# Kernel optimization log

Hardware: AMD Instinct MI355X
Metric: run time of the kernel (lower is better)

The kernel has to match this reference:

```python
import jax, jax.numpy as jnp
import numpy as np

N, E = 50000, 800000
IN_DIM, HID, HEADS, OUT_DIM = 128, 64, 4, 40
NEG_SLOPE = 0.2


def setup_inputs() -> dict:
    key = jax.random.key(0)
    ks = jax.random.split(key, 12)
    x = jax.random.normal(ks[0], (N, IN_DIM), dtype=jnp.float32)
    edge_index = jax.random.randint(ks[1], (2, E), 0, N, dtype=jnp.int64)
    timesteps = jax.random.randint(ks[2], (N,), 0, 100, dtype=jnp.int64)
    s = 1.0 / np.sqrt(IN_DIM)
    W_proj = jax.random.uniform(ks[3], (IN_DIM, HID), jnp.float32, -s, s)
    b_proj = jnp.zeros((HID,), jnp.float32)
    time_emb = jax.random.normal(ks[4], (100, HID), dtype=jnp.float32)
    sg = 1.0 / np.sqrt(HID)
    W_gat = jax.random.uniform(ks[5], (HID, HEADS * HID), jnp.float32, -sg, sg)
    att_src = jax.random.uniform(ks[6], (HEADS, HID), jnp.float32, -sg, sg)
    att_dst = jax.random.uniform(ks[7], (HEADS, HID), jnp.float32, -sg, sg)
    b_gat = jnp.zeros((HEADS * HID,), jnp.float32)
    sc = 1.0 / np.sqrt(HEADS * HID)
    W_cls = jax.random.uniform(ks[8], (HEADS * HID, OUT_DIM), jnp.float32, -sc, sc)
    b_cls = jnp.zeros((OUT_DIM,), jnp.float32)
    return {"x": x, "edge_index": edge_index, "timesteps": timesteps,
            "W_proj": W_proj, "b_proj": b_proj, "time_emb": time_emb,
            "W_gat": W_gat, "att_src": att_src, "att_dst": att_dst, "b_gat": b_gat,
            "W_cls": W_cls, "b_cls": b_cls}


def reference(x, edge_index, timesteps, W_proj, b_proj, time_emb,
              W_gat, att_src, att_dst, b_gat, W_cls, b_cls):
    n = x.shape[0]
    # feature projection + ReLU + time embedding
    h0 = jax.nn.relu(x @ W_proj + b_proj) + time_emb[timesteps]  # [N, HID]
    # --- GATConv (PyG semantics, add_self_loops=True, concat heads) ---
    h = (h0 @ W_gat).reshape(n, HEADS, HID)              # [N, H, C]
    a_src = jnp.einsum('nhc,hc->nh', h, att_src)         # [N, H]
    a_dst = jnp.einsum('nhc,hc->nh', h, att_dst)
    loops = jnp.arange(n, dtype=edge_index.dtype)
    src = jnp.concatenate([edge_index[0], loops])        # [E+N]
    dst = jnp.concatenate([edge_index[1], loops])
    e = jax.nn.leaky_relu(a_src[src] + a_dst[dst], NEG_SLOPE)  # [E+N, H]
    # segment softmax over incoming edges per destination node
    m = jax.ops.segment_max(e, dst, num_segments=n)      # [N, H]
    p = jnp.exp(e - m[dst])
    denom = jax.ops.segment_sum(p, dst, num_segments=n)  # [N, H]
    alpha = p / (denom[dst] + 1e-16)                     # [E+N, H]
    msg = alpha[:, :, None] * h[src]                     # [E+N, H, C]
    agg = jax.ops.segment_sum(msg, dst, num_segments=n)  # [N, H, C]
    gat_out = agg.reshape(n, HEADS * HID) + b_gat
    # ReLU + (dropout is identity in eval) + classifier
    return jax.nn.relu(gat_out) @ W_cls + b_cls          # [N, OUT_DIM]
```

## Files before the change

kernel.cpp:

```cpp
#include <hip/hip_runtime.h>
#include <hip/hip_fp16.h>

#define IN_DIM 128
#define HID 64
#define HEADS 4
#define OUT_DIM 40
#define CAP 64
#define NEG 0.2f
#define PA_EPB 4096
#define BKT_SH 9
#define BKT_CAP 10240
#define GPAD 264

__device__ __forceinline__ float lrelu(float v) { return v > 0.f ? v : NEG * v; }

union HU { float2 f2; __half2 h2[2]; };
union HU2 { float4 f4; __half2 h2[4]; };

typedef _Float16 h2v __attribute__((ext_vector_type(2)));
union DU { float4 f4; h2v h[4]; };

typedef _Float16 f16x8 __attribute__((ext_vector_type(8)));
typedef float f32x4 __attribute__((ext_vector_type(4)));
union FU { float4 f4; f16x8 v; };

__device__ __forceinline__ float4 unpack_h4(float2 bits) {
    HU u; u.f2 = bits;
    float2 lo = __half22float2(u.h2[0]);
    float2 hi = __half22float2(u.h2[1]);
    return make_float4(lo.x, lo.y, hi.x, hi.y);
}

__global__ __launch_bounds__(256) void partA_kernel(
    const int* __restrict__ ei, int E, int nbkt, int paBlocks,
    int* __restrict__ cnt, unsigned int* __restrict__ ebuf,
    const float* __restrict__ Wg, const float* __restrict__ attS,
    const float* __restrict__ attD, const float* __restrict__ Wc,
    float* __restrict__ aSf, float* __restrict__ aDf,
    __half* __restrict__ WgT, __half* __restrict__ WcTg)
{
    if (blockIdx.x >= paBlocks) {
        int gid = (blockIdx.x - paBlocks) * 256 + threadIdx.x;
        if (gid < 256) {
            int k = gid >> 2, hd = gid & 3;
            const float* wr = Wg + k * 256 + hd * 64;
            const float* as = attS + hd * 64;
            const float* ad = attD + hd * 64;
            float ss = 0.f, dd = 0.f;
            for (int c = 0; c < 64; ++c) { float w = wr[c]; ss += w * as[c]; dd += w * ad[c]; }
            aSf[k * 4 + hd] = ss;
            aDf[k * 4 + hd] = dd;
        } else if (gid < 256 + 256 * HID) {
            int i = gid - 256;
            int o = i >> 6, k = i & 63;
            WgT[i] = __float2half(Wg[k * 256 + o]);
        } else if (gid < 256 + 256 * HID + OUT_DIM * 256) {
            int i = gid - 256 - 256 * HID;
            int o = i >> 8, k = i & 255;
            WcTg[i] = __float2half(Wc[k * OUT_DIM + o]);
        }
        return;
    }

    __shared__ int localCnt[128];
    __shared__ int baseArr[128];
    for (int i = threadIdx.x; i < nbkt; i += 256) localCnt[i] = 0;
    __syncthreads();

    const int e0 = blockIdx.x * PA_EPB + threadIdx.x;
    unsigned short l[16];
#pragma unroll
    for (int j = 0; j < 16; ++j) {
        int e = e0 + j * 256;
        if (e < E) {
            int d = ei[E + e];
            l[j] = (unsigned short)atomicAdd(&localCnt[d >> BKT_SH], 1);
        }
    }
    __syncthreads();
    for (int i = threadIdx.x; i < nbkt; i += 256)
        baseArr[i] = atomicAdd(&cnt[i], localCnt[i]);
    __syncthreads();
#pragma unroll
    for (int j = 0; j < 16; ++j) {
        int e = e0 + j * 256;
        if (e < E) {
            int s = ei[e];
            int d = ei[E + e];
            int b = d >> BKT_SH;
            int off = baseArr[b] + (int)l[j];
            if (off < BKT_CAP)
                ebuf[(size_t)b * BKT_CAP + off] =
                    ((unsigned)(d & ((1 << BKT_SH) - 1)) << 16) | (unsigned)s;
        }
    }
}

__global__ __launch_bounds__(256) void partB_kernel(
    const unsigned int* __restrict__ ebuf, const int* __restrict__ cnt,
    int* __restrict__ deg, unsigned short* __restrict__ csr, int N)
{
    __shared__ int cntL[512];
    __shared__ unsigned short rows[512 * CAP];
    const int b = blockIdx.x;
    for (int i = threadIdx.x; i < 512; i += 256) cntL[i] = 0;
    __syncthreads();

    int cb = cnt[b]; cb = cb < BKT_CAP ? cb : BKT_CAP;
    const unsigned int* eb = ebuf + (size_t)b * BKT_CAP;
    for (int i = threadIdx.x; i < cb; i += 256) {
        unsigned v = eb[i];
        int dloc = v >> 16;
        int slot = atomicAdd(&cntL[dloc], 1);
        if (slot < CAP) rows[dloc * CAP + slot] = (unsigned short)(v & 0xFFFFu);
    }
    __syncthreads();

    const int d0 = b << BKT_SH;
    for (int i = threadIdx.x; i < 512; i += 256) {
        int d = d0 + i;
        if (d < N) deg[d] = cntL[i];
    }
    int limRows = N - d0; limRows = limRows < 512 ? limRows : 512;
    if (limRows <= 0) return;
    const uint4* rsrc = (const uint4*)rows;
    uint4* rdst = (uint4*)(csr + (size_t)d0 * CAP);
    int nvec = (limRows * CAP) >> 3;
    for (int i = threadIdx.x; i < nvec; i += 256)
        rdst[i] = rsrc[i];
}

__global__ __launch_bounds__(256) void proj_kernel(
    const float* __restrict__ x, const float* __restrict__ Wp,
    const float* __restrict__ bp, const float* __restrict__ temb,
    const int* __restrict__ ts, const float* __restrict__ aSf,
    const float* __restrict__ aDf,
    __half* __restrict__ h0h, float* __restrict__ aS, float* __restrict__ aD, int N)
{
    __shared__ __half Wl[IN_DIM * HID];
    for (int i = threadIdx.x * 8; i < IN_DIM * HID; i += 256 * 8) {
        float4 wa = *(const float4*)(Wp + i);
        float4 wb = *(const float4*)(Wp + i + 4);
        HU2 u;
        u.h2[0] = __floats2half2_rn(wa.x, wa.y);
        u.h2[1] = __floats2half2_rn(wa.z, wa.w);
        u.h2[2] = __floats2half2_rn(wb.x, wb.y);
        u.h2[3] = __floats2half2_rn(wb.z, wb.w);
        *(float4*)(Wl + i) = u.f4;
    }
    __syncthreads();

    const int t = threadIdx.x;
    const int lane = t & 63, wq = t >> 6;
    const int cg = lane & 15, ng = lane >> 4;
    const int c0 = cg * 4;
    const int nodeBase = blockIdx.x * 32 + wq * 8 + ng * 2;

    float4 acc[2];
#pragma unroll
    for (int j = 0; j < 2; ++j) acc[j] = make_float4(0.f, 0.f, 0.f, 0.f);

    for (int k0 = 0; k0 < IN_DIM; k0 += 4) {
        float4 xv[2];
#pragma unroll
        for (int j = 0; j < 2; ++j) {
            int n = nodeBase + j; n = n < N ? n : N - 1;
            xv[j] = *(const float4*)(x + (size_t)n * IN_DIM + k0);
        }
        float4 wv[4];
#pragma unroll
        for (int kk = 0; kk < 4; ++kk)
            wv[kk] = unpack_h4(*(const float2*)(Wl + (k0 + kk) * HID + c0));
#pragma unroll
        for (int j = 0; j < 2; ++j) {
            const float* xs = (const float*)&xv[j];
#pragma unroll
            for (int kk = 0; kk < 4; ++kk) {
                acc[j].x += xs[kk] * wv[kk].x;
                acc[j].y += xs[kk] * wv[kk].y;
                acc[j].z += xs[kk] * wv[kk].z;
                acc[j].w += xs[kk] * wv[kk].w;
            }
        }
    }
    const float4 bb = *(const float4*)(bp + c0);
    float4 s0 = *(const float4*)(aSf + (c0 + 0) * 4);
    float4 s1 = *(const float4*)(aSf + (c0 + 1) * 4);
    float4 s2 = *(const float4*)(aSf + (c0 + 2) * 4);
    float4 s3 = *(const float4*)(aSf + (c0 + 3) * 4);
    float4 d0 = *(const float4*)(aDf + (c0 + 0) * 4);
    float4 d1 = *(const float4*)(aDf + (c0 + 1) * 4);
    float4 d2 = *(const float4*)(aDf + (c0 + 2) * 4);
    float4 d3 = *(const float4*)(aDf + (c0 + 3) * 4);
#pragma unroll
    for (int j = 0; j < 2; ++j) {
        int n = nodeBase + j;
        float4 r = make_float4(0.f, 0.f, 0.f, 0.f);
        if (n < N) {
            int tv = ts[n];
            float4 te = *(const float4*)(temb + (size_t)tv * HID + c0);
            r.x = fmaxf(acc[j].x + bb.x, 0.f) + te.x;
            r.y = fmaxf(acc[j].y + bb.y, 0.f) + te.y;
            r.z = fmaxf(acc[j].z + bb.z, 0.f) + te.z;
            r.w = fmaxf(acc[j].w + bb.w, 0.f) + te.w;
            HU u;
            u.h2[0] = __floats2half2_rn(r.x, r.y);
            u.h2[1] = __floats2half2_rn(r.z, r.w);
            *(float2*)(h0h + (size_t)n * HID + c0) = u.f2;
        }
        float4 pS, pD;
        pS.x = r.x * s0.x + r.y * s1.x + r.z * s2.x + r.w * s3.x;
        pS.y = r.x * s0.y + r.y * s1.y + r.z * s2.y + r.w * s3.y;
        pS.z = r.x * s0.z + r.y * s1.z + r.z * s2.z + r.w * s3.z;
        pS.w = r.x * s0.w + r.y * s1.w + r.z * s2.w + r.w * s3.w;
        pD.x = r.x * d0.x + r.y * d1.x + r.z * d2.x + r.w * d3.x;
        pD.y = r.x * d0.y + r.y * d1.y + r.z * d2.y + r.w * d3.y;
        pD.z = r.x * d0.z + r.y * d1.z + r.z * d2.z + r.w * d3.z;
        pD.w = r.x * d0.w + r.y * d1.w + r.z * d2.w + r.w * d3.w;
#pragma unroll
        for (int off = 8; off > 0; off >>= 1) {
            pS.x += __shfl_down(pS.x, off); pS.y += __shfl_down(pS.y, off);
            pS.z += __shfl_down(pS.z, off); pS.w += __shfl_down(pS.w, off);
            pD.x += __shfl_down(pD.x, off); pD.y += __shfl_down(pD.y, off);
            pD.z += __shfl_down(pD.z, off); pD.w += __shfl_down(pD.w, off);
        }
        if (cg == 0 && n < N) {
            *(float4*)(aS + (size_t)n * 4) = pS;
            *(float4*)(aD + (size_t)n * 4) = pD;
        }
    }
}

__global__ __launch_bounds__(256) void agg_kernel(
    const __half* __restrict__ h0h, const float* __restrict__ aS,
    const float* __restrict__ aD, const int* __restrict__ deg,
    const unsigned short* __restrict__ csr, __half* __restrict__ agg0h, int N)
{
    __shared__ float p_lds[4 * CAP * HEADS];
    __shared__ int   s_lds[4 * CAP];

    const int t = threadIdx.x;
    const int lane = t & 63, wq = t >> 6;
    const int n = blockIdx.x * 4 + wq;
    if (n >= N) return;
    const int hd16 = lane >> 4, li = lane & 15;

    const float adn = aD[n * 4 + hd16];
    const float es = lrelu(aS[n * 4 + hd16] + adn);

    int dn = deg[n]; dn = dn < CAP ? dn : CAP;
    const unsigned short* cs = csr + (size_t)n * CAP;
    float* pL = p_lds + wq * CAP * HEADS;
    int*   sL = s_lds + wq * CAP;

    float m = -1e30f;
    for (int i = li; i < dn; i += 16) {
        int src = cs[i];
        if (hd16 == 0) sL[i] = src << 7;
        float e = lrelu(aS[src * 4 + hd16] + adn);
        pL[i * HEADS + hd16] = e;
        m = fmaxf(m, e);
    }
#pragma unroll
    for (int off = 8; off > 0; off >>= 1)
        m = fmaxf(m, __shfl_xor(m, off));
    m = fmaxf(m, es);
    float mh[4], esh[4];
#pragma unroll
    for (int h = 0; h < 4; ++h) {
        mh[h]  = __shfl(m, h * 16);
        esh[h] = __shfl(es, h * 16);
    }

    float sp = 0.f;
    for (int idx = lane; idx < dn * 4; idx += 64) {
        float p = __expf(pL[idx] - mh[idx & 3]);
        pL[idx] = p;
        sp += p;
    }
#pragma unroll
    for (int off = 4; off < 64; off <<= 1)
        sp += __shfl_xor(sp, off);
    float pselfh[4], invh[4];
#pragma unroll
    for (int h = 0; h < 4; ++h) {
        float sh = __shfl(sp, h);
        pselfh[h] = __expf(esh[h] - mh[h]);
        invh[h] = 1.f / (sh + pselfh[h] + 1e-16f);
    }

    const int half = lane >> 5;
    const int ch2 = lane & 31;
    const char* hb = (const char*)h0h;
    const int laneByte = ch2 << 2;

    float2 acc[4];
    {
        float lo = 0.f, hi = 0.f;
        if (half == 0) {
            __half2 v2 = *(const __half2*)(hb + ((size_t)n << 7) + laneByte);
            float2 f = __half22float2(v2);
            lo = f.x; hi = f.y;
        }
#pragma unroll
        for (int h = 0; h < 4; ++h) {
            acc[h].x = pselfh[h] * lo;
            acc[h].y = pselfh[h] * hi;
        }
    }
    int i = 0;
    for (; i + 8 <= dn; i += 8) {
        int off0 = sL[i + 0 + half];
        int off1 = sL[i + 2 + half];
        int off2 = sL[i + 4 + half];
        int off3 = sL[i + 6 + half];
        __half2 v0 = *(const __half2*)(hb + off0 + laneByte);
        __half2 v1 = *(const __half2*)(hb + off1 + laneByte);
        __half2 v2 = *(const __half2*)(hb + off2 + laneByte);
        __half2 v3 = *(const __half2*)(hb + off3 + laneByte);
        float4 p0 = *(const float4*)(pL + (i + 0 + half) * 4);
        float4 p1 = *(const float4*)(pL + (i + 2 + half) * 4);
        float4 p2 = *(const float4*)(pL + (i + 4 + half) * 4);
        float4 p3 = *(const float4*)(pL + (i + 6 + half) * 4);
        float2 f;
        f = __half22float2(v0);
        acc[0].x += p0.x * f.x; acc[0].y += p0.x * f.y;
        acc[1].x += p0.y * f.x; acc[1].y += p0.y * f.y;
        acc[2].x += p0.z * f.x; acc[2].y += p0.z * f.y;
        acc[3].x += p0.w * f.x; acc[3].y += p0.w * f.y;
        f = __half22float2(v1);
        acc[0].x += p1.x * f.x; acc[0].y += p1.x * f.y;
        acc[1].x += p1.y * f.x; acc[1].y += p1.y * f.y;
        acc[2].x += p1.z * f.x; acc[2].y += p1.z * f.y;
        acc[3].x += p1.w * f.x; acc[3].y += p1.w * f.y;
        f = __half22float2(v2);
        acc[0].x += p2.x * f.x; acc[0].y += p2.x * f.y;
        acc[1].x += p2.y * f.x; acc[1].y += p2.y * f.y;
        acc[2].x += p2.z * f.x; acc[2].y += p2.z * f.y;
        acc[3].x += p2.w * f.x; acc[3].y += p2.w * f.y;
        f = __half22float2(v3);
        acc[0].x += p3.x * f.x; acc[0].y += p3.x * f.y;
        acc[1].x += p3.y * f.x; acc[1].y += p3.y * f.y;
        acc[2].x += p3.z * f.x; acc[2].y += p3.z * f.y;
        acc[3].x += p3.w * f.x; acc[3].y += p3.w * f.y;
    }
    for (; i + 2 <= dn; i += 2) {
        int off0 = sL[i + half];
        __half2 v0 = *(const __half2*)(hb + off0 + laneByte);
        float4 p0 = *(const float4*)(pL + (i + half) * 4);
        float2 f = __half22float2(v0);
        acc[0].x += p0.x * f.x; acc[0].y += p0.x * f.y;
        acc[1].x += p0.y * f.x; acc[1].y += p0.y * f.y;
        acc[2].x += p0.z * f.x; acc[2].y += p0.z * f.y;
        acc[3].x += p0.w * f.x; acc[3].y += p0.w * f.y;
    }
    if (i < dn && half == 0) {
        int off0 = sL[i];
        __half2 v0 = *(const __half2*)(hb + off0 + laneByte);
        float4 p0 = *(const float4*)(pL + i * 4);
        float2 f = __half22float2(v0);
        acc[0].x += p0.x * f.x; acc[0].y += p0.x * f.y;
        acc[1].x += p0.y * f.x; acc[1].y += p0.y * f.y;
        acc[2].x += p0.z * f.x; acc[2].y += p0.z * f.y;
        acc[3].x += p0.w * f.x; acc[3].y += p0.w * f.y;
    }
#pragma unroll
    for (int h = 0; h < 4; ++h) {
        acc[h].x += __shfl_xor(acc[h].x, 32);
        acc[h].y += __shfl_xor(acc[h].y, 32);
    }
    if (lane < 32) {
        __half2* dst = (__half2*)(agg0h + (size_t)n * 256);
#pragma unroll
        for (int h = 0; h < 4; ++h)
            dst[h * 32 + ch2] = __floats2half2_rn(acc[h].x * invh[h],
                                                  acc[h].y * invh[h]);
    }
}

__global__ __launch_bounds__(256) void gatcls_kernel(
    const __half* __restrict__ agg0h, const __half* __restrict__ WgT,
    const float* __restrict__ bg, const __half* __restrict__ WcTg,
    const float* __restrict__ bc, float* __restrict__ out, int N)
{
    __shared__ __half gtile[32 * GPAD];

    const int t = threadIdx.x;
    const int lane = t & 63, wq = t >> 6;
    const int m16 = lane & 15, quad = lane >> 4;
    const int nodeBase = blockIdx.x * 32;

    {
        const int h = wq;
        f32x4 acc[2][4];
#pragma unroll
        for (int mt = 0; mt < 2; ++mt)
#pragma unroll
            for (int nt = 0; nt < 4; ++nt)
                acc[mt][nt] = (f32x4){0.f, 0.f, 0.f, 0.f};

#pragma unroll
        for (int ks = 0; ks < 2; ++ks) {
            FU a[2], b[4];
#pragma unroll
            for (int mt = 0; mt < 2; ++mt) {
                int n = nodeBase + mt * 16 + m16; n = n < N ? n : N - 1;
                a[mt].f4 = *(const float4*)(agg0h + (size_t)n * 256 + h * 64 + ks * 32 + quad * 8);
            }
#pragma unroll
            for (int nt = 0; nt < 4; ++nt) {
                int o = h * 64 + nt * 16 + m16;
                b[nt].f4 = *(const float4*)(WgT + o * 64 + ks * 32 + quad * 8);
            }
#pragma unroll
            for (int mt = 0; mt < 2; ++mt)
#pragma unroll
                for (int nt = 0; nt < 4; ++nt)
                    acc[mt][nt] = __builtin_amdgcn_mfma_f32_16x16x32_f16(
                        a[mt].v, b[nt].v, acc[mt][nt], 0, 0, 0);
        }
#pragma unroll
        for (int nt = 0; nt < 4; ++nt) {
            int o = h * 64 + nt * 16 + m16;
            float bv = bg[o];
#pragma unroll
            for (int mt = 0; mt < 2; ++mt) {
#pragma unroll
                for (int r = 0; r < 4; ++r) {
                    int nloc = mt * 16 + quad * 4 + r;
                    gtile[nloc * GPAD + o] = __float2half(fmaxf(acc[mt][nt][r] + bv, 0.f));
                }
            }
        }
    }
    __syncthreads();

    {
        const int mt = wq >> 1;
        const int ntCount = (wq & 1) ? 1 : 2;
        const int ntBase = (wq & 1) ? 2 : 0;
        f32x4 acc2[2];
        acc2[0] = (f32x4){0.f, 0.f, 0.f, 0.f};
        acc2[1] = (f32x4){0.f, 0.f, 0.f, 0.f};
#pragma unroll
        for (int ks = 0; ks < 8; ++ks) {
            FU a; a.f4 = *(const float4*)(gtile + (mt * 16 + m16) * GPAD + ks * 32 + quad * 8);
            for (int q = 0; q < ntCount; ++q) {
                int o = (ntBase + q) * 16 + m16;
                int oc = o < OUT_DIM ? o : OUT_DIM - 1;
                FU b; b.f4 = *(const float4*)(WcTg + oc * 256 + ks * 32 + quad * 8);
                acc2[q] = __builtin_amdgcn_mfma_f32_16x16x32_f16(a.v, b.v, acc2[q], 0, 0, 0);
            }
        }
        for (int q = 0; q < ntCount; ++q) {
            int o = (ntBase + q) * 16 + m16;
            if (o < OUT_DIM) {
                float bv = bc[o];
#pragma unroll
                for (int r = 0; r < 4; ++r) {
                    int n = nodeBase + mt * 16 + quad * 4 + r;
                    if (n < N) out[(size_t)n * OUT_DIM + o] = acc2[q][r] + bv;
                }
            }
        }
    }
}

extern "C" void kernel_launch(void* const* d_in, const int* in_sizes, int n_in,
                              void* d_out, int out_size, void* d_ws, size_t ws_size,
                              hipStream_t stream) {
    const float* x    = (const float*)d_in[0];
    const int*   ei   = (const int*)d_in[1];
    const int*   ts   = (const int*)d_in[2];
    const float* Wp   = (const float*)d_in[3];
    const float* bp   = (const float*)d_in[4];
    const float* temb = (const float*)d_in[5];
    const float* Wg   = (const float*)d_in[6];
    const float* attS = (const float*)d_in[7];
    const float* attD = (const float*)d_in[8];
    const float* bg   = (const float*)d_in[9];
    const float* Wc   = (const float*)d_in[10];
    const float* bc   = (const float*)d_in[11];
    float* out = (float*)d_out;

    const int N = in_sizes[0] / IN_DIM;
    const int E = in_sizes[1] / 2;
    const int nbkt = (N + (1 << BKT_SH) - 1) >> BKT_SH;

    char* w = (char*)d_ws;
    __half*         h0h   = (__half*)w;         w += (size_t)N * HID * 2;
    __half*         agg0h = (__half*)w;         w += (size_t)N * 256 * 2;
    float*          aS    = (float*)w;          w += (size_t)N * HEADS * 4;
    float*          aD    = (float*)w;          w += (size_t)N * HEADS * 4;
    int*            deg   = (int*)w;            w += (size_t)N * 4;
    unsigned short* csr   = (unsigned short*)w; w += (size_t)N * CAP * 2;
    unsigned int*   ebuf  = (unsigned int*)w;   w += (size_t)nbkt * BKT_CAP * 4;
    int*            cnt   = (int*)w;            w += (size_t)nbkt * 4;
    float*          aSf   = (float*)w;          w += 256 * 4;
    float*          aDf   = (float*)w;          w += 256 * 4;
    __half*         WgT   = (__half*)w;         w += (size_t)256 * HID * 2;
    __half*         WcTg  = (__half*)w;         w += (size_t)OUT_DIM * 256 * 2;

    const int paBlocks = (E + PA_EPB - 1) / PA_EPB;
    const int prepWork = 256 + 256 * HID + OUT_DIM * 256;
    const int prepBlocks = (prepWork + 255) / 256;

    hipMemsetAsync(cnt, 0, (size_t)nbkt * 4, stream);
    partA_kernel<<<paBlocks + prepBlocks, 256, 0, stream>>>(
        ei, E, nbkt, paBlocks, cnt, ebuf, Wg, attS, attD, Wc, aSf, aDf, WgT, WcTg);
    partB_kernel<<<nbkt, 256, 0, stream>>>(ebuf, cnt, deg, csr, N);
    proj_kernel<<<(N + 31) / 32, 256, 0, stream>>>(x, Wp, bp, temb, ts, aSf, aDf,
                                                   h0h, aS, aD, N);
    agg_kernel<<<(N + 3) / 4, 256, 0, stream>>>(h0h, aS, aD, deg, csr, agg0h, N);
    gatcls_kernel<<<(N + 31) / 32, 256, 0, stream>>>(agg0h, WgT, bg, WcTg, bc, out, N);
}
```

Measured before the change: 210.9 us.

## Fuse CSR bucket build into projection kernel and scatter CSR directly to global

Merges the CSR bucket-fill kernel and the feature projection kernel into a single launch, where the first nbkt blocks build CSR rows and the remaining blocks do the projection. The bucket blocks now write each edge's source id straight to global CSR memory instead of staging a 64KB shared-memory row buffer and copying it out. This removes one launch boundary and lets the two independent phases overlap. In exchange, CSR writes become scattered 2-byte global stores, and the merged kernel's shared-memory footprint is sized to the projection weights.

```diff
diff --git a/kernel.cpp b/kernel.cpp
--- a/kernel.cpp
+++ b/kernel.cpp
@@ -96,48 +96,42 @@
     }
 }
 
-__global__ __launch_bounds__(256) void partB_kernel(
+__global__ __launch_bounds__(256) void partBproj_kernel(
     const unsigned int* __restrict__ ebuf, const int* __restrict__ cnt,
-    int* __restrict__ deg, unsigned short* __restrict__ csr, int N)
-{
-    __shared__ int cntL[512];
-    __shared__ unsigned short rows[512 * CAP];
-    const int b = blockIdx.x;
-    for (int i = threadIdx.x; i < 512; i += 256) cntL[i] = 0;
-    __syncthreads();
-
-    int cb = cnt[b]; cb = cb < BKT_CAP ? cb : BKT_CAP;
-    const unsigned int* eb = ebuf + (size_t)b * BKT_CAP;
-    for (int i = threadIdx.x; i < cb; i += 256) {
-        unsigned v = eb[i];
-        int dloc = v >> 16;
-        int slot = atomicAdd(&cntL[dloc], 1);
-        if (slot < CAP) rows[dloc * CAP + slot] = (unsigned short)(v & 0xFFFFu);
-    }
-    __syncthreads();
-
-    const int d0 = b << BKT_SH;
-    for (int i = threadIdx.x; i < 512; i += 256) {
-        int d = d0 + i;
-        if (d < N) deg[d] = cntL[i];
-    }
-    int limRows = N - d0; limRows = limRows < 512 ? limRows : 512;
-    if (limRows <= 0) return;
-    const uint4* rsrc = (const uint4*)rows;
-    uint4* rdst = (uint4*)(csr + (size_t)d0 * CAP);
-    int nvec = (limRows * CAP) >> 3;
-    for (int i = threadIdx.x; i < nvec; i += 256)
-        rdst[i] = rsrc[i];
-}
-
-__global__ __launch_bounds__(256) void proj_kernel(
+    int* __restrict__ deg, unsigned short* __restrict__ csr, int nbkt,
     const float* __restrict__ x, const float* __restrict__ Wp,
     const float* __restrict__ bp, const float* __restrict__ temb,
     const int* __restrict__ ts, const float* __restrict__ aSf,
     const float* __restrict__ aDf,
     __half* __restrict__ h0h, float* __restrict__ aS, float* __restrict__ aD, int N)
 {
-    __shared__ __half Wl[IN_DIM * HID];
+    __shared__ __align__(16) char smem[IN_DIM * HID * 2];
+
+    if ((int)blockIdx.x < nbkt) {
+        int* cntL = (int*)smem;
+        const int b = blockIdx.x;
+        for (int i = threadIdx.x; i < 512; i += 256) cntL[i] = 0;
+        __syncthreads();
+
+        int cb = cnt[b]; cb = cb < BKT_CAP ? cb : BKT_CAP;
+        const unsigned int* eb = ebuf + (size_t)b * BKT_CAP;
+        const int d0 = b << BKT_SH;
+        for (int i = threadIdx.x; i < cb; i += 256) {
+            unsigned v = eb[i];
+            int dloc = v >> 16;
+            int slot = atomicAdd(&cntL[dloc], 1);
+            if (slot < CAP)
+                csr[((size_t)(d0 + dloc) << 6) + slot] = (unsigned short)(v & 0xFFFFu);
+        }
+        __syncthreads();
+        for (int i = threadIdx.x; i < 512; i += 256) {
+            int d = d0 + i;
+            if (d < N) deg[d] = cntL[i];
+        }
+        return;
+    }
+
+    __half* Wl = (__half*)smem;
     for (int i = threadIdx.x * 8; i < IN_DIM * HID; i += 256 * 8) {
         float4 wa = *(const float4*)(Wp + i);
         float4 wb = *(const float4*)(Wp + i + 4);
@@ -154,7 +148,7 @@
     const int lane = t & 63, wq = t >> 6;
     const int cg = lane & 15, ng = lane >> 4;
     const int c0 = cg * 4;
-    const int nodeBase = blockIdx.x * 32 + wq * 8 + ng * 2;
+    const int nodeBase = ((int)blockIdx.x - nbkt) * 32 + wq * 8 + ng * 2;
 
     float4 acc[2];
 #pragma unroll
@@ -504,13 +498,13 @@
     const int paBlocks = (E + PA_EPB - 1) / PA_EPB;
     const int prepWork = 256 + 256 * HID + OUT_DIM * 256;
     const int prepBlocks = (prepWork + 255) / 256;
+    const int projBlocks = (N + 31) / 32;
 
     hipMemsetAsync(cnt, 0, (size_t)nbkt * 4, stream);
     partA_kernel<<<paBlocks + prepBlocks, 256, 0, stream>>>(
         ei, E, nbkt, paBlocks, cnt, ebuf, Wg, attS, attD, Wc, aSf, aDf, WgT, WcTg);
-    partB_kernel<<<nbkt, 256, 0, stream>>>(ebuf, cnt, deg, csr, N);
-    proj_kernel<<<(N + 31) / 32, 256, 0, stream>>>(x, Wp, bp, temb, ts, aSf, aDf,
-                                                   h0h, aS, aD, N);
+    partBproj_kernel<<<nbkt + projBlocks, 256, 0, stream>>>(
+        ebuf, cnt, deg, csr, nbkt, x, Wp, bp, temb, ts, aSf, aDf, h0h, aS, aD, N);
     agg_kernel<<<(N + 3) / 4, 256, 0, stream>>>(h0h, aS, aD, deg, csr, agg0h, N);
     gatcls_kernel<<<(N + 31) / 32, 256, 0, stream>>>(agg0h, WgT, bg, WcTg, bc, out, N);
 }
```

After: 199.1 us. 1.06x faster.
